# Performance work log

Measured on AMD Instinct MI355X. Metric: run time of the kernel, lower is better.

Reference implementation:

```python
import jax, jax.numpy as jnp
import numpy as np

OFFS = [(0, 0), (1, 0), (-1, 0), (0, 1), (0, -1), (1, -1), (-1, 1)]  # (dq, dr)
B, H, W, E, NH, L = 16, 64, 64, 254, 8, 8
C = E + 2          # d_model = 256
DFF = 4 * C        # 1024
MLP = 512
VOCAB = 9


def setup_inputs():
    ks = jax.random.split(jax.random.key(0), 24)
    r = lambda k, s: jax.random.normal(k, s, dtype=jnp.float32) * 0.05
    return {
        'grid': jax.random.randint(ks[0], (B, H, W), 0, VOCAB),
        'gold': jax.random.normal(ks[1], (B, 2), dtype=jnp.float32),
        'emb': r(ks[2], (VOCAB, E)),
        'in_w': r(ks[3], (L, 3 * C, C)), 'in_b': r(ks[4], (L, 3 * C)),
        'out_w': r(ks[5], (L, C, C)), 'out_b': r(ks[6], (L, C)),
        'l1_w': r(ks[7], (L, DFF, C)), 'l1_b': r(ks[8], (L, DFF)),
        'l2_w': r(ks[9], (L, C, DFF)), 'l2_b': r(ks[10], (L, C)),
        'n1_g': jnp.ones((L, C)), 'n1_b': jnp.zeros((L, C)),
        'n2_g': jnp.ones((L, C)), 'n2_b': jnp.zeros((L, C)),
        'fn_g': jnp.ones((C,)), 'fn_b': jnp.zeros((C,)),
        'pw1': r(ks[11], (MLP, C)), 'pb1': r(ks[12], (MLP,)),
        'pw2': r(ks[13], (3, MLP)), 'pb2': r(ks[14], (3,)),
        'cw1': r(ks[15], (128, C)), 'cb1': r(ks[16], (128,)),
        'cw2': r(ks[17], (1, 128)), 'cb2': r(ks[18], (1,)),
    }


def _ln(x, g, b, eps=1e-5):
    m = jnp.mean(x, -1, keepdims=True)
    v = jnp.mean(jnp.square(x - m), -1, keepdims=True)
    return (x - m) * jax.lax.rsqrt(v + eps) * g + b


def _hex_gather(x):
    # x: (B,H,W,C) -> (B,H,W,7,C); out-of-bounds neighbors are zero vectors
    b, h, w, c = x.shape
    xp = jnp.pad(x, ((0, 0), (1, 1), (1, 1), (0, 0)))
    feats = [xp[:, 1 + dr:1 + dr + h, 1 + dq:1 + dq + w, :] for (dq, dr) in OFFS]
    return jnp.stack(feats, axis=3)


def _mha(x, kv, w_in, b_in, w_out, b_out):
    # x: (B,H,W,C) queries; kv: (B,H,W,7,C); full-bias projections, no mask
    c = x.shape[-1]
    hd = c // NH
    wq, wk, wv = w_in[:c], w_in[c:2 * c], w_in[2 * c:]
    bq, bk, bv = b_in[:c], b_in[c:2 * c], b_in[2 * c:]
    q = (x @ wq.T + bq).reshape(*x.shape[:-1], NH, hd)
    k = (kv @ wk.T + bk).reshape(*kv.shape[:-1], NH, hd)
    v = (kv @ wv.T + bv).reshape(*kv.shape[:-1], NH, hd)
    scores = jnp.einsum('bxyne,bxykne->bxynk', q, k) / np.sqrt(hd).astype(np.float32)
    attn = jax.nn.softmax(scores, axis=-1)
    o = jnp.einsum('bxynk,bxykne->bxyne', attn, v)
    o = o.reshape(*x.shape[:-1], c)
    return o @ w_out.T + b_out


def _pos_embed(h, w, d):
    half = d // 2
    div = jnp.exp(jnp.arange(0, half, 2, dtype=jnp.float32) * (-np.log(10000.0) / half))
    pw = jnp.arange(w, dtype=jnp.float32)[:, None] * div
    pe_w = jnp.concatenate([jnp.sin(pw), jnp.cos(pw)], -1)  # (W, 2*len(div))
    ph = jnp.arange(h, dtype=jnp.float32)[:, None] * div
    pe_h = jnp.concatenate([jnp.sin(ph), jnp.cos(ph)], -1)
    cw, ch = pe_w.shape[-1], pe_h.shape[-1]
    pe = jnp.zeros((h, w, d), dtype=jnp.float32)
    pe = pe.at[:, :, :cw].set(jnp.broadcast_to(pe_w[None, :, :], (h, w, cw)))
    pe = pe.at[:, :, cw:cw + ch].set(jnp.broadcast_to(pe_h[:, None, :], (h, w, ch)))
    return pe


def _forward(grid, gold, emb, in_w, in_b, out_w, out_b, l1_w, l1_b, l2_w, l2_b,
             n1_g, n1_b, n2_g, n2_b, fn_g, fn_b, pw1, pb1, pw2, pb2, cw1, cb1, cw2, cb2):
    b, h, w = grid.shape
    feats = jnp.concatenate(
        [emb[grid], jnp.broadcast_to(gold[:, None, None, :], (b, h, w, 2))], -1)
    x = feats + _pos_embed(h, w, C)[None]
    for i in range(L):
        kvg = _hex_gather(x)
        a = _mha(x, kvg, in_w[i], in_b[i], out_w[i], out_b[i])
        x = _ln(x + a, n1_g[i], n1_b[i])
        ff = jax.nn.relu(x @ l1_w[i].T + l1_b[i]) @ l2_w[i].T + l2_b[i]
        x = _ln(x + ff, n2_g[i], n2_b[i])
    x = _ln(x, fn_g, fn_b)
    pooled = jnp.mean(x, axis=(1, 2))  # (B,C) critic adaptive-avg-pool
    value = (jax.nn.relu(pooled @ cw1.T + cb1) @ cw2.T + cb2)[:, 0]
    pol = jax.nn.relu(x @ pw1.T + pb1) @ pw2.T + pb2  # (B,H,W,3)
    return pol[..., 2], pol[..., 0], pol[..., 1], value


def reference(grid, gold, emb, in_w, in_b, out_w, out_b, l1_w, l1_b, l2_w, l2_b,
              n1_g, n1_b, n2_g, n2_b, fn_g, fn_b, pw1, pb1, pw2, pb2, cw1, cb1, cw2, cb2):
    return _forward(grid, gold, emb, in_w, in_b, out_w, out_b, l1_w, l1_b, l2_w, l2_b,
                    n1_g, n1_b, n2_g, n2_b, fn_g, fn_b, pw1, pb1, pw2, pb2,
                    cw1, cb1, cw2, cb2)
```

## Files before the change

kernel.cpp:

```cpp
#include <hip/hip_runtime.h>

typedef __bf16 bf16x8 __attribute__((ext_vector_type(8)));
typedef float  f32x4  __attribute__((ext_vector_type(4)));
typedef unsigned short u16;
typedef u16 u16x8 __attribute__((ext_vector_type(8)));
typedef u16 u16x4 __attribute__((ext_vector_type(4)));

__device__ __forceinline__ float bf2f(u16 h) {
  union { unsigned u; float f; } w; w.u = ((unsigned)h) << 16; return w.f;
}
__device__ __forceinline__ u16 f2bf(float f) {
  union { float f; unsigned u; } w; w.f = f;
  return (u16)((w.u + 0x7fffu + ((w.u >> 16) & 1u)) >> 16);
}

__global__ __launch_bounds__(256)
void cvt_kernel(const float* __restrict__ src, u16* __restrict__ dst, int n) {
  int i = blockIdx.x * 256 + threadIdx.x;
  if (i < n) dst[i] = f2bf(src[i]);
}

__global__ __launch_bounds__(256)
void embed_kernel(const int* __restrict__ grd, const float* __restrict__ gold,
                  const float* __restrict__ emb, u16* __restrict__ xbf) {
  int t = blockIdx.x, c = threadIdx.x;
  int b = t >> 12, y = (t >> 6) & 63, xw = t & 63;
  int g = grd[t];
  float v = (c < 254) ? emb[g * 254 + c] : gold[b * 2 + (c - 254)];
  int j = c & 63;
  float dv = expf(-(float)(2 * j) * (9.210340371976184f / 128.0f));
  float arg = ((c < 128) ? (float)xw : (float)y) * dv;
  v += (c & 64) ? cosf(arg) : sinf(arg);
  xbf[(long)t * 256 + c] = f2bf(v);
}

template<int RELU, int ROWS>
__global__ __launch_bounds__(256)
void gemm_qn(const u16* __restrict__ A, const u16* __restrict__ W,
             const float* __restrict__ bias, u16* __restrict__ out,
             int Nout, int NT) {
  constexpr int NI = ROWS / 32;
  __shared__ u16 sA[ROWS * 256];
  __shared__ u16 sW[128 * 64];
  int tid = threadIdx.x;
  int lane = tid & 63, wave = tid >> 6;
  int wr = wave >> 1, wc = wave & 1;
  long rowbase = (long)blockIdx.x * ROWS;
  unsigned lbase = (unsigned)(tid & ~63) * 16;

  {
    int ac = tid & 31;
#pragma unroll
    for (int p = 0; p < ROWS / 8; ++p) {
      int row = p * 8 + (tid >> 5);
      int sc = (ac & 24) | ((ac ^ row) & 7);
      const u16* src = A + (rowbase + row) * 256 + sc * 8;
      __builtin_amdgcn_global_load_lds(
          (const __attribute__((address_space(1))) void*)src,
          (__attribute__((address_space(3))) void*)((char*)sA + p * 4096 + lbase),
          16, 0, 0);
    }
  }

  f32x4 acc[NI][4] = {};
  int T = NT * 4;
  for (int t = 0; t < T; ++t) {
    int nt = t >> 2, kc = t & 3;
    __syncthreads();
#pragma unroll
    for (int p = 0; p < 4; ++p) {
      int row = p * 32 + (tid >> 3);
      int sc = ((tid & 7) ^ row) & 7;
      const u16* src = W + (long)(nt * 128 + row) * 256 + kc * 64 + sc * 8;
      __builtin_amdgcn_global_load_lds(
          (const __attribute__((address_space(1))) void*)src,
          (__attribute__((address_space(3))) void*)((char*)sW + p * 4096 + lbase),
          16, 0, 0);
    }
    __syncthreads();

#pragma unroll
    for (int kk = 0; kk < 2; ++kk) {
      bf16x8 af[NI], bw[4];
#pragma unroll
      for (int i = 0; i < NI; ++i) {
        int ra = wr * (ROWS / 2) + i * 16 + (lane & 15);
        int l = kc * 8 + kk * 4 + (lane >> 4);
        int phys = (l & 24) | ((l ^ ra) & 7);
        af[i] = *(const bf16x8*)((const char*)sA + ra * 512 + phys * 16);
      }
#pragma unroll
      for (int j = 0; j < 4; ++j) {
        int rb = wc * 64 + j * 16 + (lane & 15);
        int m = kk * 4 + (lane >> 4);
        int phys = (m ^ rb) & 7;
        bw[j] = *(const bf16x8*)((const char*)sW + rb * 128 + phys * 16);
      }
#pragma unroll
      for (int i = 0; i < NI; ++i)
#pragma unroll
        for (int j = 0; j < 4; ++j)
          acc[i][j] = __builtin_amdgcn_mfma_f32_16x16x32_bf16(af[i], bw[j], acc[i][j], 0, 0, 0);
    }

    if (kc == 3) {
#pragma unroll
      for (int i = 0; i < NI; ++i) {
        long r0 = rowbase + wr * (ROWS / 2) + i * 16 + ((lane >> 4) * 4);
#pragma unroll
        for (int j = 0; j < 4; ++j) {
          long col = (long)nt * 128 + wc * 64 + j * 16 + (lane & 15);
          float bv = bias[col];
#pragma unroll
          for (int r = 0; r < 4; ++r) {
            float v = acc[i][j][r] + bv;
            if (RELU) v = fmaxf(v, 0.0f);
            out[(r0 + r) * Nout + col] = f2bf(v);
            acc[i][j][r] = 0.0f;
          }
        }
      }
    }
  }
}

template<int KC>
__global__ __launch_bounds__(256)
void gemm_rln(const u16* __restrict__ A, int lda, const u16* __restrict__ W,
              const float* __restrict__ bias, u16* __restrict__ xbf,
              const float* __restrict__ g, const float* __restrict__ b) {
  __shared__ __align__(16) char smem[40960];
  u16* sAr = (u16*)smem;
  u16* sWr = (u16*)(smem + 8192);
  float* red = (float*)smem;
  int tid = threadIdx.x;
  int lane = tid & 63, wave = tid >> 6;
  long rowbase = (long)blockIdx.x * 64;
  unsigned lbase = (unsigned)(tid & ~63) * 16;

  f32x4 acc[4][4] = {};
  for (int kc = 0; kc < KC; ++kc) {
    __syncthreads();
#pragma unroll
    for (int p = 0; p < 2; ++p) {
      int row = p * 32 + (tid >> 3);
      int sc = ((tid & 7) ^ row) & 7;
      const u16* src = A + (rowbase + row) * lda + kc * 64 + sc * 8;
      __builtin_amdgcn_global_load_lds(
          (const __attribute__((address_space(1))) void*)src,
          (__attribute__((address_space(3))) void*)((char*)sAr + p * 4096 + lbase),
          16, 0, 0);
    }
#pragma unroll
    for (int p = 0; p < 8; ++p) {
      int row = p * 32 + (tid >> 3);
      int sc = ((tid & 7) ^ row) & 7;
      const u16* src = W + (long)row * (KC * 64) + kc * 64 + sc * 8;
      __builtin_amdgcn_global_load_lds(
          (const __attribute__((address_space(1))) void*)src,
          (__attribute__((address_space(3))) void*)((char*)sWr + p * 4096 + lbase),
          16, 0, 0);
    }
    __syncthreads();

#pragma unroll
    for (int kk = 0; kk < 2; ++kk) {
      bf16x8 af[4], bw[4];
#pragma unroll
      for (int i = 0; i < 4; ++i) {
        int ra = i * 16 + (lane & 15);
        int m = kk * 4 + (lane >> 4);
        int phys = (m ^ ra) & 7;
        af[i] = *(const bf16x8*)((const char*)sAr + ra * 128 + phys * 16);
      }
#pragma unroll
      for (int j = 0; j < 4; ++j) {
        int rb = wave * 64 + j * 16 + (lane & 15);
        int m = kk * 4 + (lane >> 4);
        int phys = (m ^ rb) & 7;
        bw[j] = *(const bf16x8*)((const char*)sWr + rb * 128 + phys * 16);
      }
#pragma unroll
      for (int i = 0; i < 4; ++i)
#pragma unroll
        for (int j = 0; j < 4; ++j)
          acc[i][j] = __builtin_amdgcn_mfma_f32_16x16x32_bf16(af[i], bw[j], acc[i][j], 0, 0, 0);
    }
  }

  float gcol[4], bcol[4];
  long colb = wave * 64 + (lane & 15);
#pragma unroll
  for (int j = 0; j < 4; ++j) { gcol[j] = g[colb + j * 16]; bcol[j] = b[colb + j * 16]; }

  __syncthreads();

#pragma unroll
  for (int i = 0; i < 4; ++i) {
#pragma unroll
    for (int r = 0; r < 4; ++r) {
      int rowl = i * 16 + (lane >> 4) * 4 + r;
      long rbase = (rowbase + rowl) * 256;
      float ps = 0.f, pss = 0.f;
#pragma unroll
      for (int j = 0; j < 4; ++j) {
        float v = acc[i][j][r] + bias[colb + j * 16] + bf2f(xbf[rbase + colb + j * 16]);
        acc[i][j][r] = v;
        ps += v; pss += v * v;
      }
#pragma unroll
      for (int m = 1; m < 16; m <<= 1) { ps += __shfl_xor(ps, m); pss += __shfl_xor(pss, m); }
      if ((lane & 15) == 0) {
        red[wave * 64 + rowl] = ps;
        red[256 + wave * 64 + rowl] = pss;
      }
    }
  }
  __syncthreads();
  if (tid < 64) {
    float s = red[tid] + red[64 + tid] + red[128 + tid] + red[192 + tid];
    float ss = red[256 + tid] + red[320 + tid] + red[384 + tid] + red[448 + tid];
    float mean = s * (1.0f / 256.0f);
    float var = ss * (1.0f / 256.0f) - mean * mean;
    red[512 + tid * 2] = mean;
    red[512 + tid * 2 + 1] = rsqrtf(var + 1e-5f);
  }
  __syncthreads();

#pragma unroll
  for (int i = 0; i < 4; ++i) {
#pragma unroll
    for (int r = 0; r < 4; ++r) {
      int rowl = i * 16 + (lane >> 4) * 4 + r;
      float mean = red[512 + rowl * 2];
      float rstd = red[512 + rowl * 2 + 1];
      long rbase = (rowbase + rowl) * 256;
#pragma unroll
      for (int j = 0; j < 4; ++j) {
        float o = (acc[i][j][r] - mean) * rstd * gcol[j] + bcol[j];
        xbf[rbase + colb + j * 16] = f2bf(o);
      }
    }
  }
}

__global__ __launch_bounds__(256)
void attn_kernel(u16* __restrict__ qkv, const float* __restrict__ bin) {
  const int drA[7] = {0, 0, 0, 1, -1, -1, 1};
  const int dqA[7] = {0, 1, -1, 0, 0, 1, -1};
  int bid = blockIdx.x;
  int bswz = (bid & 7) * 512 + (bid >> 3);
  int gid = bswz * 256 + threadIdx.x;
  int t = gid >> 4;
  int sub = gid & 15;
  int hoff = sub * 16;
  int b = t >> 12, y = (t >> 6) & 63, xw = t & 63;
  long tbase = (long)t * 768 + hoff;

  long tn[7]; float okf[7];
#pragma unroll
  for (int n = 0; n < 7; ++n) {
    int yy = y + drA[n], xx = xw + dqA[n];
    bool ok = ((unsigned)yy < 64u) && ((unsigned)xx < 64u);
    int yc = yy < 0 ? 0 : (yy > 63 ? 63 : yy);
    int xc = xx < 0 ? 0 : (xx > 63 ? 63 : xx);
    tn[n] = ((long)(b * 4096 + yc * 64 + xc)) * 768 + hoff;
    okf[n] = ok ? 1.0f : 0.0f;
  }

  u16x8 qraw[2], kr[7][2];
  {
    const u16x8* qp = (const u16x8*)(qkv + tbase);
    qraw[0] = qp[0]; qraw[1] = qp[1];
  }
#pragma unroll
  for (int n = 0; n < 7; ++n) {
    const u16x8* kp = (const u16x8*)(qkv + tn[n] + 256);
    kr[n][0] = kp[0]; kr[n][1] = kp[1];
  }

  float q[16];
#pragma unroll
  for (int j = 0; j < 2; ++j)
#pragma unroll
    for (int e = 0; e < 8; ++e) q[j * 8 + e] = bf2f(qraw[j][e]);

  float skb = 0.f;
  {
    const float* kb = bin + 256 + hoff;
#pragma unroll
    for (int i = 0; i < 16; ++i) skb += q[i] * kb[i];
  }

  float s[7];
#pragma unroll
  for (int n = 0; n < 7; ++n) {
    float acc = 0.f;
#pragma unroll
    for (int j = 0; j < 2; ++j)
#pragma unroll
      for (int e = 0; e < 8; ++e) acc += q[j * 8 + e] * bf2f(kr[n][j][e]);
    float p = (okf[n] != 0.f) ? acc : skb;
    p += __shfl_xor(p, 1);
    s[n] = p * 0.17677669529663687f;
  }

  u16x8 vr[7][2];
#pragma unroll
  for (int n = 0; n < 7; ++n) {
    const u16x8* vp = (const u16x8*)(qkv + tn[n] + 512);
    vr[n][0] = vp[0]; vr[n][1] = vp[1];
  }

  float mx = s[0];
#pragma unroll
  for (int n = 1; n < 7; ++n) mx = fmaxf(mx, s[n]);
  float wsum = 0.0f;
#pragma unroll
  for (int n = 0; n < 7; ++n) { s[n] = expf(s[n] - mx); wsum += s[n]; }
  float inv = 1.0f / wsum;

  float o[16];
#pragma unroll
  for (int i = 0; i < 16; ++i) o[i] = 0.0f;
  float woob = 0.f;
#pragma unroll
  for (int n = 0; n < 7; ++n) {
    float wk = okf[n] * s[n];
    woob += s[n] - wk;
#pragma unroll
    for (int j = 0; j < 2; ++j)
#pragma unroll
      for (int e = 0; e < 8; ++e) o[j * 8 + e] += wk * bf2f(vr[n][j][e]);
  }
  {
    const float* vb = bin + 512 + hoff;
#pragma unroll
    for (int i = 0; i < 16; ++i) o[i] += woob * vb[i];
  }

  u16x8* op = (u16x8*)(qkv + tbase);
#pragma unroll
  for (int j = 0; j < 2; ++j) {
    u16x8 ov;
#pragma unroll
    for (int e = 0; e < 8; ++e) ov[e] = f2bf(o[j * 8 + e] * inv);
    op[j] = ov;
  }
}

__global__ __launch_bounds__(256)
void ln_kernel(u16* __restrict__ xbf, const float* __restrict__ g,
               const float* __restrict__ b) {
  int wave = threadIdx.x >> 6, lane = threadIdx.x & 63;
  long t = (long)blockIdx.x * 4 + wave;
  long base = t * 256 + lane * 4;
  u16x4 raw = *(const u16x4*)(xbf + base);
  float v0 = bf2f(raw[0]), v1 = bf2f(raw[1]), v2 = bf2f(raw[2]), v3 = bf2f(raw[3]);
  float s = v0 + v1 + v2 + v3;
  float ss = v0 * v0 + v1 * v1 + v2 * v2 + v3 * v3;
#pragma unroll
  for (int m = 1; m < 64; m <<= 1) { s += __shfl_xor(s, m); ss += __shfl_xor(ss, m); }
  float mean = s * (1.0f / 256.0f);
  float var = ss * (1.0f / 256.0f) - mean * mean;
  float rstd = rsqrtf(var + 1e-5f);
  float4 gv = *(const float4*)(g + lane * 4);
  float4 bv = *(const float4*)(b + lane * 4);
  u16x4 ob;
  ob[0] = f2bf((v0 - mean) * rstd * gv.x + bv.x);
  ob[1] = f2bf((v1 - mean) * rstd * gv.y + bv.y);
  ob[2] = f2bf((v2 - mean) * rstd * gv.z + bv.z);
  ob[3] = f2bf((v3 - mean) * rstd * gv.w + bv.w);
  *(u16x4*)(xbf + base) = ob;
}

__global__ __launch_bounds__(256)
void pol2_kernel(const u16* __restrict__ h, const float* __restrict__ pw2,
                 const float* __restrict__ pb2, float* __restrict__ out) {
  __shared__ float sw[1536];
  int tid = threadIdx.x;
  for (int i = tid; i < 1536; i += 256) sw[i] = pw2[i];
  __syncthreads();
  int wave = tid >> 6, lane = tid & 63;
  long t = (long)blockIdx.x * 4 + wave;
  long hb = t * 512 + lane * 8;
  float a0 = 0.f, a1 = 0.f, a2 = 0.f;
#pragma unroll
  for (int e = 0; e < 8; ++e) {
    float hv = bf2f(h[hb + e]);
    int le = lane * 8 + e;
    a0 += hv * sw[le];
    a1 += hv * sw[512 + le];
    a2 += hv * sw[1024 + le];
  }
#pragma unroll
  for (int m = 1; m < 64; m <<= 1) {
    a0 += __shfl_xor(a0, m); a1 += __shfl_xor(a1, m); a2 += __shfl_xor(a2, m);
  }
  if (lane == 0) {
    out[t]           = a2 + pb2[2];
    out[65536 + t]   = a0 + pb2[0];
    out[131072 + t]  = a1 + pb2[1];
  }
}

__global__ __launch_bounds__(256)
void pool1_kernel(const u16* __restrict__ xbf, float* __restrict__ part) {
  int bid = blockIdx.x, c = threadIdx.x;
  long base = (long)bid * 128 * 256;
  float s = 0.f;
  for (int p = 0; p < 128; ++p) s += bf2f(xbf[base + (long)p * 256 + c]);
  part[(long)bid * 256 + c] = s;
}
__global__ __launch_bounds__(256)
void pool2_kernel(const float* __restrict__ part, float* __restrict__ pooled) {
  int b = blockIdx.x, c = threadIdx.x;
  float s = 0.f;
  for (int seg = 0; seg < 32; ++seg) s += part[((long)b * 32 + seg) * 256 + c];
  pooled[b * 256 + c] = s * (1.0f / 4096.0f);
}

__global__ __launch_bounds__(128)
void value_kernel(const float* __restrict__ pooled, const float* __restrict__ cw1,
                  const float* __restrict__ cb1, const float* __restrict__ cw2,
                  const float* __restrict__ cb2, float* __restrict__ out) {
  int b = blockIdx.x, j = threadIdx.x;
  __shared__ float red[2];
  float hj = cb1[j];
  const float* pr = pooled + b * 256;
  const float* wr = cw1 + j * 256;
  for (int c = 0; c < 256; ++c) hj += pr[c] * wr[c];
  hj = fmaxf(hj, 0.0f);
  float acc = hj * cw2[j];
#pragma unroll
  for (int m = 1; m < 64; m <<= 1) acc += __shfl_xor(acc, m);
  if ((j & 63) == 0) red[j >> 6] = acc;
  __syncthreads();
  if (j == 0) out[196608 + b] = red[0] + red[1] + cb2[0];
}

extern "C" void kernel_launch(void* const* d_in, const int* in_sizes, int n_in,
                              void* d_out, int out_size, void* d_ws, size_t ws_size,
                              hipStream_t stream) {
  const int*   grd  = (const int*)d_in[0];
  const float* gold = (const float*)d_in[1];
  const float* emb  = (const float*)d_in[2];
  const float* in_w = (const float*)d_in[3];
  const float* in_b = (const float*)d_in[4];
  const float* out_w= (const float*)d_in[5];
  const float* out_b= (const float*)d_in[6];
  const float* l1_w = (const float*)d_in[7];
  const float* l1_b = (const float*)d_in[8];
  const float* l2_w = (const float*)d_in[9];
  const float* l2_b = (const float*)d_in[10];
  const float* n1_g = (const float*)d_in[11];
  const float* n1_b = (const float*)d_in[12];
  const float* n2_g = (const float*)d_in[13];
  const float* n2_b = (const float*)d_in[14];
  const float* fn_g = (const float*)d_in[15];
  const float* fn_b = (const float*)d_in[16];
  const float* pw1  = (const float*)d_in[17];
  const float* pb1  = (const float*)d_in[18];
  const float* pw2  = (const float*)d_in[19];
  const float* pb2  = (const float*)d_in[20];
  const float* cw1  = (const float*)d_in[21];
  const float* cb1  = (const float*)d_in[22];
  const float* cw2  = (const float*)d_in[23];
  const float* cb2  = (const float*)d_in[24];
  float* out = (float*)d_out;

  char* ws = (char*)d_ws;
  u16*   xbf    = (u16*)ws;
  char*  region = ws + (32l << 20);
  u16*   qkv    = (u16*)region;
  u16*   hbuf   = (u16*)region;
  u16*   wbf    = (u16*)(ws + (160l << 20));
  float* part   = (float*)(ws + (173l << 20));
  float* pooled = (float*)(ws + (174l << 20));

  u16* inw_bf  = wbf;
  u16* outw_bf = inw_bf + 1572864;
  u16* l1w_bf  = outw_bf + 524288;
  u16* l2w_bf  = l1w_bf + 2097152;
  u16* pw1_bf  = l2w_bf + 2097152;

  cvt_kernel<<<(1572864 + 255) / 256, 256, 0, stream>>>(in_w, inw_bf, 1572864);
  cvt_kernel<<<(524288 + 255) / 256, 256, 0, stream>>>(out_w, outw_bf, 524288);
  cvt_kernel<<<(2097152 + 255) / 256, 256, 0, stream>>>(l1_w, l1w_bf, 2097152);
  cvt_kernel<<<(2097152 + 255) / 256, 256, 0, stream>>>(l2_w, l2w_bf, 2097152);
  cvt_kernel<<<(131072 + 255) / 256, 256, 0, stream>>>(pw1, pw1_bf, 131072);

  embed_kernel<<<65536, 256, 0, stream>>>(grd, gold, emb, xbf);

  for (int i = 0; i < 8; ++i) {
    gemm_qn<0, 128><<<512, 256, 0, stream>>>(
        xbf, inw_bf + (long)i * 196608, in_b + i * 768, qkv, 768, 6);
    attn_kernel<<<4096, 256, 0, stream>>>(qkv, in_b + i * 768);
    gemm_rln<4><<<1024, 256, 0, stream>>>(
        qkv, 768, outw_bf + (long)i * 65536, out_b + i * 256, xbf,
        n1_g + i * 256, n1_b + i * 256);
    gemm_qn<1, 64><<<1024, 256, 0, stream>>>(
        xbf, l1w_bf + (long)i * 262144, l1_b + i * 1024, hbuf, 1024, 8);
    gemm_rln<16><<<1024, 256, 0, stream>>>(
        hbuf, 1024, l2w_bf + (long)i * 262144, l2_b + i * 256, xbf,
        n2_g + i * 256, n2_b + i * 256);
  }

  ln_kernel<<<16384, 256, 0, stream>>>(xbf, fn_g, fn_b);

  gemm_qn<1, 128><<<512, 256, 0, stream>>>(xbf, pw1_bf, pb1, hbuf, 512, 4);
  pol2_kernel<<<16384, 256, 0, stream>>>(hbuf, pw2, pb2, out);

  pool1_kernel<<<512, 256, 0, stream>>>(xbf, part);
  pool2_kernel<<<16, 256, 0, stream>>>(part, pooled);
  value_kernel<<<16, 128, 0, stream>>>(pooled, cw1, cb1, cw2, cb2, out);
}
```

Before: 2.044 ms.

## Fuse policy head MLP into single GEMM kernel and retile FFN1 GEMM

Replaces the policy-head pw1 GEMM plus the separate pol2 reduction kernel with one kernel. It computes relu(x@pw1+b1) in registers and reduces it directly against pw2 using shuffles and shared-memory partial sums, so the 64K×512 hidden buffer is never written to or read back from global memory. The FFN first GEMM is also switched from 64-row tiles over 1024 blocks to 128-row tiles over 512 blocks. The larger tile gives more reuse per block but halves the number of blocks available for parallelism.

```diff
diff --git a/kernel.cpp b/kernel.cpp
--- a/kernel.cpp
+++ b/kernel.cpp
@@ -121,6 +121,117 @@
         }
       }
     }
+  }
+}
+
+__global__ __launch_bounds__(256)
+void gemm_pol(const u16* __restrict__ A, const u16* __restrict__ W,
+              const float* __restrict__ b1, const float* __restrict__ pw2,
+              const float* __restrict__ pb2, float* __restrict__ out) {
+  __shared__ u16 sA[64 * 256];
+  __shared__ u16 sW[128 * 64];
+  __shared__ float part[2][3][64];
+  int tid = threadIdx.x;
+  int lane = tid & 63, wave = tid >> 6;
+  int wr = wave >> 1, wc = wave & 1;
+  long rowbase = (long)blockIdx.x * 64;
+  unsigned lbase = (unsigned)(tid & ~63) * 16;
+
+  for (int i = tid; i < 384; i += 256) ((float*)part)[i] = 0.0f;
+
+  {
+    int ac = tid & 31;
+#pragma unroll
+    for (int p = 0; p < 8; ++p) {
+      int row = p * 8 + (tid >> 5);
+      int sc = (ac & 24) | ((ac ^ row) & 7);
+      const u16* src = A + (rowbase + row) * 256 + sc * 8;
+      __builtin_amdgcn_global_load_lds(
+          (const __attribute__((address_space(1))) void*)src,
+          (__attribute__((address_space(3))) void*)((char*)sA + p * 4096 + lbase),
+          16, 0, 0);
+    }
+  }
+
+  f32x4 acc[2][4] = {};
+  for (int t = 0; t < 16; ++t) {
+    int nt = t >> 2, kc = t & 3;
+    __syncthreads();
+#pragma unroll
+    for (int p = 0; p < 4; ++p) {
+      int row = p * 32 + (tid >> 3);
+      int sc = ((tid & 7) ^ row) & 7;
+      const u16* src = W + (long)(nt * 128 + row) * 256 + kc * 64 + sc * 8;
+      __builtin_amdgcn_global_load_lds(
+          (const __attribute__((address_space(1))) void*)src,
+          (__attribute__((address_space(3))) void*)((char*)sW + p * 4096 + lbase),
+          16, 0, 0);
+    }
+    __syncthreads();
+
+#pragma unroll
+    for (int kk = 0; kk < 2; ++kk) {
+      bf16x8 af[2], bw[4];
+#pragma unroll
+      for (int i = 0; i < 2; ++i) {
+        int ra = wr * 32 + i * 16 + (lane & 15);
+        int l = kc * 8 + kk * 4 + (lane >> 4);
+        int phys = (l & 24) | ((l ^ ra) & 7);
+        af[i] = *(const bf16x8*)((const char*)sA + ra * 512 + phys * 16);
+      }
+#pragma unroll
+      for (int j = 0; j < 4; ++j) {
+        int rb = wc * 64 + j * 16 + (lane & 15);
+        int m = kk * 4 + (lane >> 4);
+        int phys = (m ^ rb) & 7;
+        bw[j] = *(const bf16x8*)((const char*)sW + rb * 128 + phys * 16);
+      }
+#pragma unroll
+      for (int i = 0; i < 2; ++i)
+#pragma unroll
+        for (int j = 0; j < 4; ++j)
+          acc[i][j] = __builtin_amdgcn_mfma_f32_16x16x32_bf16(af[i], bw[j], acc[i][j], 0, 0, 0);
+    }
+
+    if (kc == 3) {
+#pragma unroll
+      for (int i = 0; i < 2; ++i) {
+#pragma unroll
+        for (int r = 0; r < 4; ++r) {
+          float p0 = 0.f, p1 = 0.f, p2 = 0.f;
+#pragma unroll
+          for (int j = 0; j < 4; ++j) {
+            int col = nt * 128 + wc * 64 + j * 16 + (lane & 15);
+            float v = fmaxf(acc[i][j][r] + b1[col], 0.0f);
+            p0 += v * pw2[col];
+            p1 += v * pw2[512 + col];
+            p2 += v * pw2[1024 + col];
+            acc[i][j][r] = 0.0f;
+          }
+#pragma unroll
+          for (int m = 1; m < 16; m <<= 1) {
+            p0 += __shfl_xor(p0, m); p1 += __shfl_xor(p1, m); p2 += __shfl_xor(p2, m);
+          }
+          if ((lane & 15) == 0) {
+            int row = wr * 32 + i * 16 + (lane >> 4) * 4 + r;
+            part[wc][0][row] += p0;
+            part[wc][1][row] += p1;
+            part[wc][2][row] += p2;
+          }
+        }
+      }
+    }
+  }
+
+  __syncthreads();
+  if (tid < 64) {
+    long t = rowbase + tid;
+    float a0 = part[0][0][tid] + part[1][0][tid];
+    float a1 = part[0][1][tid] + part[1][1][tid];
+    float a2 = part[0][2][tid] + part[1][2][tid];
+    out[t]          = a2 + pb2[2];
+    out[65536 + t]  = a0 + pb2[0];
+    out[131072 + t] = a1 + pb2[1];
   }
 }
 
@@ -372,36 +483,6 @@
   ob[2] = f2bf((v2 - mean) * rstd * gv.z + bv.z);
   ob[3] = f2bf((v3 - mean) * rstd * gv.w + bv.w);
   *(u16x4*)(xbf + base) = ob;
-}
-
-__global__ __launch_bounds__(256)
-void pol2_kernel(const u16* __restrict__ h, const float* __restrict__ pw2,
-                 const float* __restrict__ pb2, float* __restrict__ out) {
-  __shared__ float sw[1536];
-  int tid = threadIdx.x;
-  for (int i = tid; i < 1536; i += 256) sw[i] = pw2[i];
-  __syncthreads();
-  int wave = tid >> 6, lane = tid & 63;
-  long t = (long)blockIdx.x * 4 + wave;
-  long hb = t * 512 + lane * 8;
-  float a0 = 0.f, a1 = 0.f, a2 = 0.f;
-#pragma unroll
-  for (int e = 0; e < 8; ++e) {
-    float hv = bf2f(h[hb + e]);
-    int le = lane * 8 + e;
-    a0 += hv * sw[le];
-    a1 += hv * sw[512 + le];
-    a2 += hv * sw[1024 + le];
-  }
-#pragma unroll
-  for (int m = 1; m < 64; m <<= 1) {
-    a0 += __shfl_xor(a0, m); a1 += __shfl_xor(a1, m); a2 += __shfl_xor(a2, m);
-  }
-  if (lane == 0) {
-    out[t]           = a2 + pb2[2];
-    out[65536 + t]   = a0 + pb2[0];
-    out[131072 + t]  = a1 + pb2[1];
-  }
 }
 
 __global__ __launch_bounds__(256)
@@ -499,7 +580,7 @@
     gemm_rln<4><<<1024, 256, 0, stream>>>(
         qkv, 768, outw_bf + (long)i * 65536, out_b + i * 256, xbf,
         n1_g + i * 256, n1_b + i * 256);
-    gemm_qn<1, 64><<<1024, 256, 0, stream>>>(
+    gemm_qn<1, 128><<<512, 256, 0, stream>>>(
         xbf, l1w_bf + (long)i * 262144, l1_b + i * 1024, hbuf, 1024, 8);
     gemm_rln<16><<<1024, 256, 0, stream>>>(
         hbuf, 1024, l2w_bf + (long)i * 262144, l2_b + i * 256, xbf,
@@ -508,8 +589,7 @@
 
   ln_kernel<<<16384, 256, 0, stream>>>(xbf, fn_g, fn_b);
 
-  gemm_qn<1, 128><<<512, 256, 0, stream>>>(xbf, pw1_bf, pb1, hbuf, 512, 4);
-  pol2_kernel<<<16384, 256, 0, stream>>>(hbuf, pw2, pb2, out);
+  gemm_pol<<<1024, 256, 0, stream>>>(xbf, pw1_bf, pb1, pw2, pb2, out);
 
   pool1_kernel<<<512, 256, 0, stream>>>(xbf, part);
   pool2_kernel<<<16, 256, 0, stream>>>(part, pooled);
```

Measured after the change: 1.923 ms, median of 2. 1.06x faster.
